# Kernel optimization log

Measured on AMD Instinct MI355X. Metric: run time of the kernel, lower is better.

The kernel has to match this reference:

```python
import math
import jax, jax.numpy as jnp
import numpy as np

H = 8
C_HIDDEN = 32
C_Q = 256


def setup_inputs() -> dict:
    key = jax.random.key(0)
    ks = jax.random.split(key, 9)
    B, S, Q, K = 1, 128, 256, 256
    q_x = jax.random.normal(ks[0], (B, S, Q, C_Q), dtype=jnp.float32)
    kv_x = jax.random.normal(ks[1], (B, S, K, C_Q), dtype=jnp.float32)
    bias1 = jax.random.normal(ks[2], (B, S, 1, 1, K), dtype=jnp.float32)
    bias2 = jax.random.normal(ks[3], (B, 1, H, Q, K), dtype=jnp.float32)
    scale = 1.0 / math.sqrt(C_Q)
    wq = jax.random.normal(ks[4], (H * C_HIDDEN, C_Q), dtype=jnp.float32) * scale
    wk = jax.random.normal(ks[5], (H * C_HIDDEN, C_Q), dtype=jnp.float32) * scale
    wv = jax.random.normal(ks[6], (H * C_HIDDEN, C_Q), dtype=jnp.float32) * scale
    wg = jax.random.normal(ks[7], (H * C_HIDDEN, C_Q), dtype=jnp.float32) * scale
    wo = jax.random.normal(ks[8], (C_Q, H * C_HIDDEN), dtype=jnp.float32) * scale
    return {"q_x": q_x, "kv_x": kv_x, "bias1": bias1, "bias2": bias2,
            "wq": wq, "wk": wk, "wv": wv, "wg": wg, "wo": wo}


def _split_heads(x):
    # [..., L, H*c] -> [..., H, L, c]
    y = x.reshape(x.shape[:-1] + (H, C_HIDDEN))
    return jnp.moveaxis(y, -2, -3)


def reference(q_x, kv_x, bias1, bias2, wq, wk, wv, wg, wo):
    # QKV projections (no bias), per-head split, scale q by 1/sqrt(c_hidden)
    q = _split_heads(q_x @ wq.T) / math.sqrt(C_HIDDEN)   # [B,S,H,Q,c]
    k = _split_heads(kv_x @ wk.T)                         # [B,S,H,K,c]
    v = _split_heads(kv_x @ wv.T)                         # [B,S,H,K,c]
    # attention logits with additive biases folded in
    a = jnp.einsum('...hqc,...hkc->...hqk', q, k) + bias1 + bias2
    a = jax.nn.softmax(a, axis=-1)
    o = jnp.einsum('...hqk,...hkc->...hqc', a, v)         # [B,S,H,Q,c]
    o = jnp.moveaxis(o, -3, -2)                           # [B,S,Q,H,c]
    # sigmoid gating from query data
    g = jax.nn.sigmoid(q_x @ wg.T)                        # [B,S,Q,H*c]
    g = g.reshape(g.shape[:-1] + (H, C_HIDDEN))
    o = o * g
    o = o.reshape(o.shape[:-2] + (H * C_HIDDEN,))         # flatten heads
    return o @ wo.T                                       # [B,S,Q,C_Q]
```

## Files before the change

kernel.cpp:

```cpp
#include <hip/hip_runtime.h>
#include <math.h>

#define S_DIM 128
#define H_DIM 8
#define M_TOT (S_DIM * 256)

typedef unsigned short ushort_t;
typedef unsigned int   uint32;
typedef __bf16  v8bf  __attribute__((ext_vector_type(8)));
typedef float   v4f   __attribute__((ext_vector_type(4)));

#define LOG2E 1.4426950408889634f

__device__ inline ushort_t f2b(float x) {
    unsigned int u = __float_as_uint(x);
    u += 0x7fffu + ((u >> 16) & 1u);
    return (ushort_t)(u >> 16);
}
__device__ inline float b2f(ushort_t h) {
    return __uint_as_float(((unsigned int)h) << 16);
}
__device__ inline uint32 packsplit(float x) {
    uint32 u = __float_as_uint(x);
    uint32 r = u + 0x7fffu + ((u >> 16) & 1u);
    float resid = x - __uint_as_float(r & 0xffff0000u);
    uint32 v = __float_as_uint(resid);
    return (r >> 16) | ((v + 0x7fffu + ((v >> 16) & 1u)) & 0xffff0000u);
}

union u4bf8 { uint4 u; v8bf v; };

__device__ inline void unpack8(const uint32* p, v8bf& hi, v8bf& lo) {
    uint4 a = *(const uint4*)p;
    uint4 b = *(const uint4*)(p + 4);
    u4bf8 h, l;
    h.u.x = __builtin_amdgcn_perm(a.y, a.x, 0x05040100u);
    h.u.y = __builtin_amdgcn_perm(a.w, a.z, 0x05040100u);
    h.u.z = __builtin_amdgcn_perm(b.y, b.x, 0x05040100u);
    h.u.w = __builtin_amdgcn_perm(b.w, b.z, 0x05040100u);
    l.u.x = __builtin_amdgcn_perm(a.y, a.x, 0x07060302u);
    l.u.y = __builtin_amdgcn_perm(a.w, a.z, 0x07060302u);
    l.u.z = __builtin_amdgcn_perm(b.y, b.x, 0x07060302u);
    l.u.w = __builtin_amdgcn_perm(b.w, b.z, 0x07060302u);
    hi = h.v; lo = l.v;
}

#define GLDS16(gp, lp) __builtin_amdgcn_global_load_lds( \
    (const __attribute__((address_space(1))) void*)(gp), \
    (__attribute__((address_space(3))) void*)(lp), 16, 0, 0)

__global__ __launch_bounds__(256) void split_f32(
    const float* __restrict__ x, ushort_t* __restrict__ hi,
    ushort_t* __restrict__ lo, int n4)
{
    int i = blockIdx.x * 256 + threadIdx.x;
    if (i >= n4) return;
    float4 v = ((const float4*)x)[i];
    ushort4 h, l;
    h.x = f2b(v.x); l.x = f2b(v.x - b2f(h.x));
    h.y = f2b(v.y); l.y = f2b(v.y - b2f(h.y));
    h.z = f2b(v.z); l.z = f2b(v.z - b2f(h.z));
    h.w = f2b(v.w); l.w = f2b(v.w - b2f(h.w));
    ((ushort4*)hi)[i] = h;
    ((ushort4*)lo)[i] = l;
}

__global__ __launch_bounds__(256) void split_w(
    const float* __restrict__ w0, const float* __restrict__ w1,
    const float* __restrict__ w2, const float* __restrict__ w3,
    const float* __restrict__ w4,
    ushort_t* __restrict__ hi, ushort_t* __restrict__ lo)
{
    const float* src;
    switch (blockIdx.y) {
        case 0: src = w0; break; case 1: src = w1; break;
        case 2: src = w2; break; case 3: src = w3; break;
        default: src = w4; break;
    }
    int i = blockIdx.x * 256 + threadIdx.x;
    float4 v = ((const float4*)src)[i];
    ushort4 h, l;
    h.x = f2b(v.x); l.x = f2b(v.x - b2f(h.x));
    h.y = f2b(v.y); l.y = f2b(v.y - b2f(h.y));
    h.z = f2b(v.z); l.z = f2b(v.z - b2f(h.z));
    h.w = f2b(v.w); l.w = f2b(v.w - b2f(h.w));
    size_t base = (size_t)blockIdx.y * 16384;
    ((ushort4*)hi)[base + i] = h;
    ((ushort4*)lo)[base + i] = l;
}

__global__ __launch_bounds__(256) void gemm_proj(
    const ushort_t* __restrict__ Ahi, const ushort_t* __restrict__ Alo,
    const ushort_t* __restrict__ Whi, const ushort_t* __restrict__ Wlo,
    uint32* __restrict__ pk_out, float* __restrict__ f32_out,
    uint32* __restrict__ pkT_out, float scale_lo, int kind)
{
    __shared__ ushort_t lds[4][128 * 32];

    const int t    = threadIdx.x;
    const int l    = t & 63;
    const int wv   = t >> 6;
    const int wm   = wv & 1;
    const int wn   = wv >> 1;
    const int idx  = l & 15;
    const int quad = l >> 4;
    const int m0   = blockIdx.y * 128;
    const int n0   = blockIdx.x * 128;

    const ushort_t* srcs[4] = { Ahi + (size_t)m0 * 256, Alo + (size_t)m0 * 256,
                                Whi + (size_t)n0 * 256, Wlo + (size_t)n0 * 256 };

    v4f acc[4][4];
    #pragma unroll
    for (int i = 0; i < 4; ++i)
        #pragma unroll
        for (int j = 0; j < 4; ++j) acc[i][j] = (v4f){0.f, 0.f, 0.f, 0.f};

    for (int k0 = 0; k0 < 256; k0 += 32) {
        #pragma unroll
        for (int b = 0; b < 4; ++b) {
            #pragma unroll
            for (int i = 0; i < 2; ++i) {
                const int sb   = wv * 128 + i * 64;
                const int slot = sb + l;
                const ushort_t* g = srcs[b] + (size_t)(slot >> 2) * 256 + k0 + (slot & 3) * 8;
                GLDS16(g, &lds[b][sb * 8]);
            }
        }
        __builtin_amdgcn_s_waitcnt(0);
        __syncthreads();

        v8bf ah[4], al[4], bh[4], bl[4];
        #pragma unroll
        for (int mt = 0; mt < 4; ++mt) {
            const int r   = wm * 64 + mt * 16 + idx;
            const int off = (r * 4 + quad) * 8;
            ah[mt] = *(const v8bf*)&lds[0][off];
            al[mt] = *(const v8bf*)&lds[1][off];
        }
        #pragma unroll
        for (int nt = 0; nt < 4; ++nt) {
            const int r   = wn * 64 + nt * 16 + idx;
            const int off = (r * 4 + quad) * 8;
            bh[nt] = *(const v8bf*)&lds[2][off];
            bl[nt] = *(const v8bf*)&lds[3][off];
        }

        #pragma unroll
        for (int mt = 0; mt < 4; ++mt)
            #pragma unroll
            for (int nt = 0; nt < 4; ++nt) {
                acc[mt][nt] = __builtin_amdgcn_mfma_f32_16x16x32_bf16(ah[mt], bh[nt], acc[mt][nt], 0, 0, 0);
                acc[mt][nt] = __builtin_amdgcn_mfma_f32_16x16x32_bf16(al[mt], bh[nt], acc[mt][nt], 0, 0, 0);
                acc[mt][nt] = __builtin_amdgcn_mfma_f32_16x16x32_bf16(ah[mt], bl[nt], acc[mt][nt], 0, 0, 0);
            }
        __syncthreads();
    }

    #pragma unroll
    for (int mt = 0; mt < 4; ++mt) {
        const int mbase = m0 + wm * 64 + mt * 16 + quad * 4;
        const int s = mbase >> 8, r8 = mbase & 255;
        #pragma unroll
        for (int nt = 0; nt < 4; ++nt) {
            const int gcol = n0 + wn * 64 + nt * 16 + idx;
            if (gcol < 256) {
                const int hh = gcol >> 5, c = gcol & 31;
                const size_t di = (((size_t)(s * 8 + hh) * 256) + r8) * 32 + c;
                #pragma unroll
                for (int r = 0; r < 4; ++r)
                    pk_out[di + (size_t)r * 32] = packsplit(acc[mt][nt][r] * scale_lo);
            } else if (kind == 0) {
                const int gc = gcol - 256;
                #pragma unroll
                for (int r = 0; r < 4; ++r)
                    f32_out[(size_t)(mbase + r) * 256 + gc] = acc[mt][nt][r];
            } else {
                const int gc = gcol - 256, hh = gc >> 5, c = gc & 31;
                uint4 pkv;
                pkv.x = packsplit(acc[mt][nt][0]);
                pkv.y = packsplit(acc[mt][nt][1]);
                pkv.z = packsplit(acc[mt][nt][2]);
                pkv.w = packsplit(acc[mt][nt][3]);
                *(uint4*)&pkT_out[(((size_t)(s * 8 + hh) * 32) + c) * 256 + r8] = pkv;
            }
        }
    }
}

__global__ __launch_bounds__(256) void gemm_split_mfma(
    const ushort_t* __restrict__ Ahi, const ushort_t* __restrict__ Alo,
    const ushort_t* __restrict__ Whi, const ushort_t* __restrict__ Wlo,
    float* __restrict__ Cf)
{
    __shared__ ushort_t lds[4][128 * 32];

    const int t    = threadIdx.x;
    const int l    = t & 63;
    const int wv   = t >> 6;
    const int wm   = wv & 1;
    const int wn   = wv >> 1;
    const int idx  = l & 15;
    const int quad = l >> 4;
    const int m0   = blockIdx.y * 128;
    const int n0   = blockIdx.x * 128;

    const ushort_t* srcs[4] = { Ahi + (size_t)m0 * 256, Alo + (size_t)m0 * 256,
                                Whi + (size_t)n0 * 256, Wlo + (size_t)n0 * 256 };

    v4f acc[4][4];
    #pragma unroll
    for (int i = 0; i < 4; ++i)
        #pragma unroll
        for (int j = 0; j < 4; ++j) acc[i][j] = (v4f){0.f, 0.f, 0.f, 0.f};

    for (int k0 = 0; k0 < 256; k0 += 32) {
        #pragma unroll
        for (int b = 0; b < 4; ++b) {
            #pragma unroll
            for (int i = 0; i < 2; ++i) {
                const int sb   = wv * 128 + i * 64;
                const int slot = sb + l;
                const ushort_t* g = srcs[b] + (size_t)(slot >> 2) * 256 + k0 + (slot & 3) * 8;
                GLDS16(g, &lds[b][sb * 8]);
            }
        }
        __builtin_amdgcn_s_waitcnt(0);
        __syncthreads();

        v8bf ah[4], al[4], bh[4], bl[4];
        #pragma unroll
        for (int mt = 0; mt < 4; ++mt) {
            const int r   = wm * 64 + mt * 16 + idx;
            const int off = (r * 4 + quad) * 8;
            ah[mt] = *(const v8bf*)&lds[0][off];
            al[mt] = *(const v8bf*)&lds[1][off];
        }
        #pragma unroll
        for (int nt = 0; nt < 4; ++nt) {
            const int r   = wn * 64 + nt * 16 + idx;
            const int off = (r * 4 + quad) * 8;
            bh[nt] = *(const v8bf*)&lds[2][off];
            bl[nt] = *(const v8bf*)&lds[3][off];
        }

        #pragma unroll
        for (int mt = 0; mt < 4; ++mt)
            #pragma unroll
            for (int nt = 0; nt < 4; ++nt) {
                acc[mt][nt] = __builtin_amdgcn_mfma_f32_16x16x32_bf16(ah[mt], bh[nt], acc[mt][nt], 0, 0, 0);
                acc[mt][nt] = __builtin_amdgcn_mfma_f32_16x16x32_bf16(al[mt], bh[nt], acc[mt][nt], 0, 0, 0);
                acc[mt][nt] = __builtin_amdgcn_mfma_f32_16x16x32_bf16(ah[mt], bl[nt], acc[mt][nt], 0, 0, 0);
            }
        __syncthreads();
    }

    #pragma unroll
    for (int mt = 0; mt < 4; ++mt) {
        #pragma unroll
        for (int nt = 0; nt < 4; ++nt) {
            const int gcol = n0 + wn * 64 + nt * 16 + idx;
            #pragma unroll
            for (int r = 0; r < 4; ++r) {
                const int grow = m0 + wm * 64 + mt * 16 + quad * 4 + r;
                Cf[(size_t)grow * 256 + gcol] = acc[mt][nt][r];
            }
        }
    }
}

__global__ __launch_bounds__(256, 2) void attn_mfma(
    const uint32* __restrict__ qpk, const uint32* __restrict__ kpk,
    const uint32* __restrict__ vpk,
    const float* __restrict__ b1, const float* __restrict__ b2,
    const float* __restrict__ gbuf,
    ushort_t* __restrict__ oh, ushort_t* __restrict__ ol)
{
    __shared__ __align__(16) uint32 pbuf[4][64 * 36];
    __shared__ __align__(16) float  lbuf[4][64 * 4];
    __shared__ __align__(16) float  invl[4][64];

    const int sh = blockIdx.x, s = sh >> 3, h = sh & 7;
    const int t = threadIdx.x, l = t & 63, w = t >> 6;
    const int idx = l & 15, quad = l >> 4;

    const size_t shb = (size_t)sh * 8192;
    const uint32* qp = qpk + shb;
    const uint32* kp = kpk + shb;
    const uint32* vp = vpk + shb;
    const float* b1p = b1 + (size_t)s * 256;
    const float* b2p = b2 + (size_t)h * 65536;

    v8bf qfh[4], qfl[4];
    #pragma unroll
    for (int nt = 0; nt < 4; ++nt)
        unpack8(qp + (w * 64 + nt * 16 + idx) * 32 + quad * 8, qfh[nt], qfl[nt]);

    v4f oacc[4][2];
    #pragma unroll
    for (int mt = 0; mt < 4; ++mt) {
        oacc[mt][0] = (v4f){0.f, 0.f, 0.f, 0.f};
        oacc[mt][1] = (v4f){0.f, 0.f, 0.f, 0.f};
    }
    float lrun[4] = {0.f, 0.f, 0.f, 0.f};

    for (int c4 = 0; c4 < 4; ++c4) {
        const int ak0 = c4 * 64;

        v8bf kfh[4], kfl[4];
        #pragma unroll
        for (int at = 0; at < 4; ++at)
            unpack8(kp + (ak0 + at * 16 + idx) * 32 + quad * 8, kfh[at], kfl[at]);

        v4f sacc[4][4];
        #pragma unroll
        for (int at = 0; at < 4; ++at)
            #pragma unroll
            for (int nt = 0; nt < 4; ++nt)
                sacc[at][nt] = (v4f){0.f, 0.f, 0.f, 0.f};
        #pragma unroll
        for (int at = 0; at < 4; ++at)
            #pragma unroll
            for (int nt = 0; nt < 4; ++nt) {
                sacc[at][nt] = __builtin_amdgcn_mfma_f32_16x16x32_bf16(kfh[at], qfh[nt], sacc[at][nt], 0, 0, 0);
                sacc[at][nt] = __builtin_amdgcn_mfma_f32_16x16x32_bf16(kfl[at], qfh[nt], sacc[at][nt], 0, 0, 0);
                sacc[at][nt] = __builtin_amdgcn_mfma_f32_16x16x32_bf16(kfh[at], qfl[nt], sacc[at][nt], 0, 0, 0);
            }

        v4f b1v[4];
        #pragma unroll
        for (int at = 0; at < 4; ++at)
            b1v[at] = *(const v4f*)(b1p + ak0 + at * 16 + quad * 4);

        #pragma unroll
        for (int at = 0; at < 4; ++at)
            #pragma unroll
            for (int nt = 0; nt < 4; ++nt) {
                const int q = w * 64 + nt * 16 + idx;
                v4f b2v = *(const v4f*)(b2p + (size_t)q * 256 + ak0 + at * 16 + quad * 4);
                float e0 = exp2f(fmaf(b1v[at][0] + b2v[0], LOG2E, sacc[at][nt][0]));
                float e1 = exp2f(fmaf(b1v[at][1] + b2v[1], LOG2E, sacc[at][nt][1]));
                float e2 = exp2f(fmaf(b1v[at][2] + b2v[2], LOG2E, sacc[at][nt][2]));
                float e3 = exp2f(fmaf(b1v[at][3] + b2v[3], LOG2E, sacc[at][nt][3]));
                lrun[nt] += (e0 + e1) + (e2 + e3);
                uint32 p0 = __builtin_amdgcn_perm(__float_as_uint(e1) + 0x8000u,
                                                  __float_as_uint(e0) + 0x8000u, 0x07060302u);
                uint32 p1 = __builtin_amdgcn_perm(__float_as_uint(e3) + 0x8000u,
                                                  __float_as_uint(e2) + 0x8000u, 0x07060302u);
                const int dw = (nt * 16 + idx) * 36 + at * 8 + quad * 2;
                *(uint2*)&pbuf[w][dw] = make_uint2(p0, p1);
            }

        v8bf vfh[2][2], vfl[2][2];
        #pragma unroll
        for (int n2 = 0; n2 < 2; ++n2)
            #pragma unroll
            for (int kt = 0; kt < 2; ++kt)
                unpack8(vp + (n2 * 16 + idx) * 256 + ak0 + kt * 32 + quad * 8,
                        vfh[n2][kt], vfl[n2][kt]);

        #pragma unroll
        for (int mt = 0; mt < 4; ++mt)
            #pragma unroll
            for (int kt = 0; kt < 2; ++kt) {
                v8bf pf = *(const v8bf*)&pbuf[w][(mt * 16 + idx) * 36 + kt * 16 + quad * 4];
                #pragma unroll
                for (int n2 = 0; n2 < 2; ++n2) {
                    oacc[mt][n2] = __builtin_amdgcn_mfma_f32_16x16x32_bf16(pf, vfh[n2][kt], oacc[mt][n2], 0, 0, 0);
                    oacc[mt][n2] = __builtin_amdgcn_mfma_f32_16x16x32_bf16(pf, vfl[n2][kt], oacc[mt][n2], 0, 0, 0);
                }
            }
    }

    #pragma unroll
    for (int nt = 0; nt < 4; ++nt)
        lbuf[w][(nt * 16 + idx) * 4 + quad] = lrun[nt];
    {
        v4f lv = *(const v4f*)&lbuf[w][l * 4];
        invl[w][l] = 1.f / ((lv[0] + lv[1]) + (lv[2] + lv[3]));
    }

    #pragma unroll
    for (int mt = 0; mt < 4; ++mt) {
        v4f iv = *(const v4f*)&invl[w][mt * 16 + quad * 4];
        #pragma unroll
        for (int n2 = 0; n2 < 2; ++n2) {
            const int c = n2 * 16 + idx;
            #pragma unroll
            for (int r = 0; r < 4; ++r) {
                const int q = w * 64 + mt * 16 + quad * 4 + r;
                const size_t gi = (size_t)(s * 256 + q) * 256 + h * 32 + c;
                const float gv = gbuf[gi];
                const float sig = 1.f / (1.f + __expf(-gv));
                const float val = oacc[mt][n2][r] * iv[r] * sig;
                const ushort_t hv = f2b(val);
                oh[gi] = hv;
                ol[gi] = f2b(val - b2f(hv));
            }
        }
    }
}

extern "C" void kernel_launch(void* const* d_in, const int* in_sizes, int n_in,
                              void* d_out, int out_size, void* d_ws, size_t ws_size,
                              hipStream_t stream)
{
    const float* q_x   = (const float*)d_in[0];
    const float* kv_x  = (const float*)d_in[1];
    const float* bias1 = (const float*)d_in[2];
    const float* bias2 = (const float*)d_in[3];
    const float* wq    = (const float*)d_in[4];
    const float* wk    = (const float*)d_in[5];
    const float* wv    = (const float*)d_in[6];
    const float* wg    = (const float*)d_in[7];
    const float* wo    = (const float*)d_in[8];
    float* out = (float*)d_out;

    const size_t BUF = (size_t)M_TOT * 256;

    float*    g_buf = (float*)d_ws;
    uint32*   qpk   = (uint32*)(g_buf + BUF);
    uint32*   kpk   = qpk + BUF;
    uint32*   vpk   = kpk + BUF;
    ushort_t* ohb   = (ushort_t*)(vpk + BUF);
    ushort_t* olb   = ohb + BUF;
    ushort_t* xhb   = olb + BUF;
    ushort_t* xlb   = xhb + BUF;
    ushort_t* w_hi  = xlb + BUF;
    ushort_t* w_lo  = w_hi + 5 * 65536;

    const float qscale = 0.17677669529663689f * LOG2E;
    const int   N4 = (int)(BUF / 4);

    split_w<<<dim3(64, 5), 256, 0, stream>>>(wq, wg, wk, wv, wo, w_hi, w_lo);

    dim3 gp(4, 256);
    dim3 gf(2, 256);

    split_f32<<<8192, 256, 0, stream>>>(q_x, xhb, xlb, N4);
    gemm_proj<<<gp, 256, 0, stream>>>(xhb, xlb, w_hi, w_lo,
                                      qpk, g_buf, nullptr, qscale, 0);

    split_f32<<<8192, 256, 0, stream>>>(kv_x, xhb, xlb, N4);
    gemm_proj<<<gp, 256, 0, stream>>>(xhb, xlb, w_hi + 2 * 65536, w_lo + 2 * 65536,
                                      kpk, nullptr, vpk, 1.f, 1);

    attn_mfma<<<S_DIM * H_DIM, 256, 0, stream>>>(
        qpk, kpk, vpk, bias1, bias2, g_buf, ohb, olb);

    gemm_split_mfma<<<gf, 256, 0, stream>>>(ohb, olb, w_hi + 4 * 65536, w_lo + 4 * 65536, out);
}
```

Baseline: 322.6 us.

## Batch Q and KV projections in one launch and store hi/lo bf16 planes separately

The two input-split kernels become one 2-D launch, and the two projection GEMMs become a single launch with a z dimension selecting the Q/G or K/V path. Projected Q, K and V are now stored as separate bf16 hi and lo planes instead of packed 32-bit hi/lo words. This lets the attention kernel load MFMA fragments directly, with no perm-based unpacking. The softmax exponent now uses __expf on the summed logits instead of exp2f with log2e folded into an fma, so the Q scale no longer carries the log2e factor. The goal is fewer launches, better GPU fill for the projections, and fewer ALU ops in the attention inner loop, at the cost of a larger workspace and one extra multiply per exponent.

```diff
diff --git a/kernel.cpp b/kernel.cpp
--- a/kernel.cpp
+++ b/kernel.cpp
@@ -10,8 +10,6 @@
 typedef __bf16  v8bf  __attribute__((ext_vector_type(8)));
 typedef float   v4f   __attribute__((ext_vector_type(4)));
 
-#define LOG2E 1.4426950408889634f
-
 __device__ inline ushort_t f2b(float x) {
     unsigned int u = __float_as_uint(x);
     u += 0x7fffu + ((u >> 16) & 1u);
@@ -20,49 +18,27 @@
 __device__ inline float b2f(ushort_t h) {
     return __uint_as_float(((unsigned int)h) << 16);
 }
-__device__ inline uint32 packsplit(float x) {
-    uint32 u = __float_as_uint(x);
-    uint32 r = u + 0x7fffu + ((u >> 16) & 1u);
-    float resid = x - __uint_as_float(r & 0xffff0000u);
-    uint32 v = __float_as_uint(resid);
-    return (r >> 16) | ((v + 0x7fffu + ((v >> 16) & 1u)) & 0xffff0000u);
-}
-
-union u4bf8 { uint4 u; v8bf v; };
-
-__device__ inline void unpack8(const uint32* p, v8bf& hi, v8bf& lo) {
-    uint4 a = *(const uint4*)p;
-    uint4 b = *(const uint4*)(p + 4);
-    u4bf8 h, l;
-    h.u.x = __builtin_amdgcn_perm(a.y, a.x, 0x05040100u);
-    h.u.y = __builtin_amdgcn_perm(a.w, a.z, 0x05040100u);
-    h.u.z = __builtin_amdgcn_perm(b.y, b.x, 0x05040100u);
-    h.u.w = __builtin_amdgcn_perm(b.w, b.z, 0x05040100u);
-    l.u.x = __builtin_amdgcn_perm(a.y, a.x, 0x07060302u);
-    l.u.y = __builtin_amdgcn_perm(a.w, a.z, 0x07060302u);
-    l.u.z = __builtin_amdgcn_perm(b.y, b.x, 0x07060302u);
-    l.u.w = __builtin_amdgcn_perm(b.w, b.z, 0x07060302u);
-    hi = h.v; lo = l.v;
-}
 
 #define GLDS16(gp, lp) __builtin_amdgcn_global_load_lds( \
     (const __attribute__((address_space(1))) void*)(gp), \
     (__attribute__((address_space(3))) void*)(lp), 16, 0, 0)
 
-__global__ __launch_bounds__(256) void split_f32(
-    const float* __restrict__ x, ushort_t* __restrict__ hi,
-    ushort_t* __restrict__ lo, int n4)
-{
+__global__ __launch_bounds__(256) void split_x(
+    const float* __restrict__ xq, const float* __restrict__ xkv,
+    ushort_t* __restrict__ hi, ushort_t* __restrict__ lo)
+{
+    const size_t BUF4 = (size_t)M_TOT * 64;
+    const float* src = blockIdx.y ? xkv : xq;
+    size_t base = (size_t)blockIdx.y * BUF4;
     int i = blockIdx.x * 256 + threadIdx.x;
-    if (i >= n4) return;
-    float4 v = ((const float4*)x)[i];
+    float4 v = ((const float4*)src)[i];
     ushort4 h, l;
     h.x = f2b(v.x); l.x = f2b(v.x - b2f(h.x));
     h.y = f2b(v.y); l.y = f2b(v.y - b2f(h.y));
     h.z = f2b(v.z); l.z = f2b(v.z - b2f(h.z));
     h.w = f2b(v.w); l.w = f2b(v.w - b2f(h.w));
-    ((ushort4*)hi)[i] = h;
-    ((ushort4*)lo)[i] = l;
+    ((ushort4*)hi)[base + i] = h;
+    ((ushort4*)lo)[base + i] = l;
 }
 
 __global__ __launch_bounds__(256) void split_w(
@@ -90,13 +66,17 @@
 }
 
 __global__ __launch_bounds__(256) void gemm_proj(
-    const ushort_t* __restrict__ Ahi, const ushort_t* __restrict__ Alo,
-    const ushort_t* __restrict__ Whi, const ushort_t* __restrict__ Wlo,
-    uint32* __restrict__ pk_out, float* __restrict__ f32_out,
-    uint32* __restrict__ pkT_out, float scale_lo, int kind)
+    const ushort_t* __restrict__ Xhi, const ushort_t* __restrict__ Xlo,
+    const ushort_t* __restrict__ Whi4, const ushort_t* __restrict__ Wlo4,
+    ushort_t* __restrict__ qh, ushort_t* __restrict__ ql,
+    ushort_t* __restrict__ kh, ushort_t* __restrict__ kl,
+    float* __restrict__ g_out,
+    ushort_t* __restrict__ vh, ushort_t* __restrict__ vl,
+    float qscale)
 {
     __shared__ ushort_t lds[4][128 * 32];
 
+    const int z    = blockIdx.z;
     const int t    = threadIdx.x;
     const int l    = t & 63;
     const int wv   = t >> 6;
@@ -107,6 +87,13 @@
     const int m0   = blockIdx.y * 128;
     const int n0   = blockIdx.x * 128;
 
+    const size_t BUF = (size_t)M_TOT * 256;
+    const ushort_t* Ahi = Xhi + (size_t)z * BUF;
+    const ushort_t* Alo = Xlo + (size_t)z * BUF;
+    const ushort_t* Whi = Whi4 + (size_t)z * 131072;
+    const ushort_t* Wlo = Wlo4 + (size_t)z * 131072;
+    const float scale = z ? 1.f : qscale;
+
     const ushort_t* srcs[4] = { Ahi + (size_t)m0 * 256, Alo + (size_t)m0 * 256,
                                 Whi + (size_t)n0 * 256, Wlo + (size_t)n0 * 256 };
 
@@ -156,6 +143,9 @@
             }
         __syncthreads();
     }
+
+    ushort_t* dsth = z ? kh : qh;
+    ushort_t* dstl = z ? kl : ql;
 
     #pragma unroll
     for (int mt = 0; mt < 4; ++mt) {
@@ -168,21 +158,30 @@
                 const int hh = gcol >> 5, c = gcol & 31;
                 const size_t di = (((size_t)(s * 8 + hh) * 256) + r8) * 32 + c;
                 #pragma unroll
-                for (int r = 0; r < 4; ++r)
-                    pk_out[di + (size_t)r * 32] = packsplit(acc[mt][nt][r] * scale_lo);
-            } else if (kind == 0) {
+                for (int r = 0; r < 4; ++r) {
+                    const float val = acc[mt][nt][r] * scale;
+                    const ushort_t hv = f2b(val);
+                    dsth[di + (size_t)r * 32] = hv;
+                    dstl[di + (size_t)r * 32] = f2b(val - b2f(hv));
+                }
+            } else if (z == 0) {
                 const int gc = gcol - 256;
                 #pragma unroll
                 for (int r = 0; r < 4; ++r)
-                    f32_out[(size_t)(mbase + r) * 256 + gc] = acc[mt][nt][r];
+                    g_out[(size_t)(mbase + r) * 256 + gc] = acc[mt][nt][r];
             } else {
                 const int gc = gcol - 256, hh = gc >> 5, c = gc & 31;
-                uint4 pkv;
-                pkv.x = packsplit(acc[mt][nt][0]);
-                pkv.y = packsplit(acc[mt][nt][1]);
-                pkv.z = packsplit(acc[mt][nt][2]);
-                pkv.w = packsplit(acc[mt][nt][3]);
-                *(uint4*)&pkT_out[(((size_t)(s * 8 + hh) * 32) + c) * 256 + r8] = pkv;
+                ushort4 hv4, lv4;
+                #pragma unroll
+                for (int r = 0; r < 4; ++r) {
+                    const float val = acc[mt][nt][r];
+                    const ushort_t hv = f2b(val);
+                    ((ushort_t*)&hv4)[r] = hv;
+                    ((ushort_t*)&lv4)[r] = f2b(val - b2f(hv));
+                }
+                const size_t di = (((size_t)(s * 8 + hh) * 32) + c) * 256 + r8;
+                *(ushort4*)&vh[di] = hv4;
+                *(ushort4*)&vl[di] = lv4;
             }
         }
     }
@@ -270,8 +269,9 @@
 }
 
 __global__ __launch_bounds__(256, 2) void attn_mfma(
-    const uint32* __restrict__ qpk, const uint32* __restrict__ kpk,
-    const uint32* __restrict__ vpk,
+    const ushort_t* __restrict__ qh, const ushort_t* __restrict__ ql,
+    const ushort_t* __restrict__ kh, const ushort_t* __restrict__ kl,
+    const ushort_t* __restrict__ vth, const ushort_t* __restrict__ vtl,
     const float* __restrict__ b1, const float* __restrict__ b2,
     const float* __restrict__ gbuf,
     ushort_t* __restrict__ oh, ushort_t* __restrict__ ol)
@@ -285,16 +285,22 @@
     const int idx = l & 15, quad = l >> 4;
 
     const size_t shb = (size_t)sh * 8192;
-    const uint32* qp = qpk + shb;
-    const uint32* kp = kpk + shb;
-    const uint32* vp = vpk + shb;
+    const ushort_t* qhp = qh + shb;
+    const ushort_t* qlp = ql + shb;
+    const ushort_t* khp = kh + shb;
+    const ushort_t* klp = kl + shb;
+    const ushort_t* vhp = vth + shb;
+    const ushort_t* vlp = vtl + shb;
     const float* b1p = b1 + (size_t)s * 256;
     const float* b2p = b2 + (size_t)h * 65536;
 
     v8bf qfh[4], qfl[4];
     #pragma unroll
-    for (int nt = 0; nt < 4; ++nt)
-        unpack8(qp + (w * 64 + nt * 16 + idx) * 32 + quad * 8, qfh[nt], qfl[nt]);
+    for (int nt = 0; nt < 4; ++nt) {
+        const int off = (w * 64 + nt * 16 + idx) * 32 + quad * 8;
+        qfh[nt] = *(const v8bf*)(qhp + off);
+        qfl[nt] = *(const v8bf*)(qlp + off);
+    }
 
     v4f oacc[4][2];
     #pragma unroll
@@ -309,8 +315,11 @@
 
         v8bf kfh[4], kfl[4];
         #pragma unroll
-        for (int at = 0; at < 4; ++at)
-            unpack8(kp + (ak0 + at * 16 + idx) * 32 + quad * 8, kfh[at], kfl[at]);
+        for (int at = 0; at < 4; ++at) {
+            const int off = (ak0 + at * 16 + idx) * 32 + quad * 8;
+            kfh[at] = *(const v8bf*)(khp + off);
+            kfl[at] = *(const v8bf*)(klp + off);
+        }
 
         v4f sacc[4][4];
         #pragma unroll
@@ -338,10 +347,10 @@
             for (int nt = 0; nt < 4; ++nt) {
                 const int q = w * 64 + nt * 16 + idx;
                 v4f b2v = *(const v4f*)(b2p + (size_t)q * 256 + ak0 + at * 16 + quad * 4);
-                float e0 = exp2f(fmaf(b1v[at][0] + b2v[0], LOG2E, sacc[at][nt][0]));
-                float e1 = exp2f(fmaf(b1v[at][1] + b2v[1], LOG2E, sacc[at][nt][1]));
-                float e2 = exp2f(fmaf(b1v[at][2] + b2v[2], LOG2E, sacc[at][nt][2]));
-                float e3 = exp2f(fmaf(b1v[at][3] + b2v[3], LOG2E, sacc[at][nt][3]));
+                float e0 = __expf(b1v[at][0] + b2v[0] + sacc[at][nt][0]);
+                float e1 = __expf(b1v[at][1] + b2v[1] + sacc[at][nt][1]);
+                float e2 = __expf(b1v[at][2] + b2v[2] + sacc[at][nt][2]);
+                float e3 = __expf(b1v[at][3] + b2v[3] + sacc[at][nt][3]);
                 lrun[nt] += (e0 + e1) + (e2 + e3);
                 uint32 p0 = __builtin_amdgcn_perm(__float_as_uint(e1) + 0x8000u,
                                                   __float_as_uint(e0) + 0x8000u, 0x07060302u);
@@ -355,9 +364,11 @@
         #pragma unroll
         for (int n2 = 0; n2 < 2; ++n2)
             #pragma unroll
-            for (int kt = 0; kt < 2; ++kt)
-                unpack8(vp + (n2 * 16 + idx) * 256 + ak0 + kt * 32 + quad * 8,
-                        vfh[n2][kt], vfl[n2][kt]);
+            for (int kt = 0; kt < 2; ++kt) {
+                const int off = (n2 * 16 + idx) * 256 + ak0 + kt * 32 + quad * 8;
+                vfh[n2][kt] = *(const v8bf*)(vhp + off);
+                vfl[n2][kt] = *(const v8bf*)(vlp + off);
+            }
 
         #pragma unroll
         for (int mt = 0; mt < 4; ++mt)
@@ -419,34 +430,27 @@
     const size_t BUF = (size_t)M_TOT * 256;
 
     float*    g_buf = (float*)d_ws;
-    uint32*   qpk   = (uint32*)(g_buf + BUF);
-    uint32*   kpk   = qpk + BUF;
-    uint32*   vpk   = kpk + BUF;
-    ushort_t* ohb   = (ushort_t*)(vpk + BUF);
-    ushort_t* olb   = ohb + BUF;
-    ushort_t* xhb   = olb + BUF;
-    ushort_t* xlb   = xhb + BUF;
-    ushort_t* w_hi  = xlb + BUF;
-    ushort_t* w_lo  = w_hi + 5 * 65536;
-
-    const float qscale = 0.17677669529663689f * LOG2E;
-    const int   N4 = (int)(BUF / 4);
+    ushort_t* p     = (ushort_t*)(g_buf + BUF);
+    ushort_t* qhb = p;            ushort_t* qlb = qhb + BUF;
+    ushort_t* khb = qlb + BUF;    ushort_t* klb = khb + BUF;
+    ushort_t* vhb = klb + BUF;    ushort_t* vlb = vhb + BUF;
+    ushort_t* ohb = vlb + BUF;    ushort_t* olb = ohb + BUF;
+    ushort_t* xhb = olb + BUF;    ushort_t* xlb = xhb + 2 * BUF;
+    ushort_t* w_hi = xlb + 2 * BUF;
+    ushort_t* w_lo = w_hi + 5 * 65536;
+
+    const float qscale = 0.17677669529663689f;
 
     split_w<<<dim3(64, 5), 256, 0, stream>>>(wq, wg, wk, wv, wo, w_hi, w_lo);
 
-    dim3 gp(4, 256);
-    dim3 gf(2, 256);
-
-    split_f32<<<8192, 256, 0, stream>>>(q_x, xhb, xlb, N4);
-    gemm_proj<<<gp, 256, 0, stream>>>(xhb, xlb, w_hi, w_lo,
-                                      qpk, g_buf, nullptr, qscale, 0);
-
-    split_f32<<<8192, 256, 0, stream>>>(kv_x, xhb, xlb, N4);
-    gemm_proj<<<gp, 256, 0, stream>>>(xhb, xlb, w_hi + 2 * 65536, w_lo + 2 * 65536,
-                                      kpk, nullptr, vpk, 1.f, 1);
+    split_x<<<dim3(8192, 2), 256, 0, stream>>>(q_x, kv_x, xhb, xlb);
+
+    gemm_proj<<<dim3(4, 256, 2), 256, 0, stream>>>(
+        xhb, xlb, w_hi, w_lo, qhb, qlb, khb, klb, g_buf, vhb, vlb, qscale);
 
     attn_mfma<<<S_DIM * H_DIM, 256, 0, stream>>>(
-        qpk, kpk, vpk, bias1, bias2, g_buf, ohb, olb);
-
-    gemm_split_mfma<<<gf, 256, 0, stream>>>(ohb, olb, w_hi + 4 * 65536, w_lo + 4 * 65536, out);
-}
+        qhb, qlb, khb, klb, vhb, vlb, bias1, bias2, g_buf, ohb, olb);
+
+    gemm_split_mfma<<<dim3(2, 256), 256, 0, stream>>>(
+        ohb, olb, w_hi + 4 * 65536, w_lo + 4 * 65536, out);
+}
```

After: 312.2 us. -3.2%, faster.
